# Kernel tuning notes

Hardware: AMD Instinct MI355X
Metric: run time of the kernel (lower is better)

## Reference

```python
import jax, jax.numpy as jnp
import numpy as np

KERNEL_MUL = 2.0
KERNEL_NUM = 5
FIX_SIGMA = None


def setup_inputs() -> dict:
    key = jax.random.key(0)
    k1, k2 = jax.random.split(key)
    source = jax.random.normal(k1, (4096, 64), dtype=jnp.float32)
    target = jax.random.normal(k2, (4096, 64), dtype=jnp.float32)
    return {"source": source, "target": target}


def reference(source, target):
    batch_size = source.shape[0]
    total = jnp.concatenate([source, target], axis=0)  # [2N, D]
    n_samples = total.shape[0]
    sq = jnp.sum(total * total, axis=1)  # [2N]
    L2 = sq[:, None] + sq[None, :] - 2.0 * (total @ total.T)  # [2N, 2N]
    if FIX_SIGMA:
        bandwidth = jnp.asarray(FIX_SIGMA, dtype=L2.dtype)
    else:
        # torch uses L2_distance.data -> detached; no grad through bandwidth
        bandwidth = jax.lax.stop_gradient(jnp.sum(L2)) / (n_samples ** 2 - n_samples)
    bandwidth = bandwidth / (KERNEL_MUL ** (KERNEL_NUM // 2))
    kernels = jnp.zeros_like(L2)
    for i in range(KERNEL_NUM):  # small fixed loop over bandwidths
        kernels = kernels + jnp.exp(-L2 / (bandwidth * (KERNEL_MUL ** i)))
    XX = kernels[:batch_size, :batch_size]
    YY = kernels[batch_size:, batch_size:]
    XY = kernels[:batch_size, batch_size:]
    YX = kernels[batch_size:, :batch_size]
    return jnp.mean(XX + YY - XY - YX)
```

## Files before the change

### kernel.cpp

```cpp
#include <hip/hip_runtime.h>
#include <math.h>

#define N_TOTAL 8192
#define BATCH   4096
#define DIMS    64
#define P1_BLOCKS 256
#define SEG     8
#define NSEG    16
#define NPART   2048


#if defined(__has_builtin)
#if __has_builtin(__builtin_amdgcn_exp2f)
#define EXP2F(x) __builtin_amdgcn_exp2f(x)
#endif
#endif
#ifndef EXP2F
#define EXP2F(x) exp2f(x)
#endif

typedef __attribute__((ext_vector_type(8))) short bf16x8;
typedef __attribute__((ext_vector_type(4))) float f32x4;
typedef __attribute__((ext_vector_type(4))) short s16x4;

__device__ inline short f2bf_rn(float x) {
    unsigned u = __float_as_uint(x);
    unsigned r = (u + 0x7fffu + ((u >> 16) & 1u)) >> 16;
    return (short)r;
}

__global__ __launch_bounds__(256) void pass1_kernel(const float* __restrict__ src,
                                                    const float* __restrict__ tgt,
                                                    double* __restrict__ sqpart,
                                                    double* __restrict__ colpart,
                                                    float* __restrict__ sqbuf,
                                                    short* __restrict__ Xh) {
    __shared__ double cred[4][64];
    __shared__ double sred[4];
    const int lane = threadIdx.x & 63;
    const int wv = threadIdx.x >> 6;
    const int sub = lane >> 4;
    const int k4 = (lane & 15) << 2;
    const int gw = blockIdx.x * 4 + wv;
    const int numWaves = P1_BLOCKS * 4;

    double colacc[4] = {0.0, 0.0, 0.0, 0.0};
    double sqacc = 0.0;

    for (int g = gw; g < N_TOTAL / 4; g += numWaves) {
        int r = g * 4 + sub;
        const float* row = (r < BATCH) ? (src + (size_t)r * DIMS)
                                       : (tgt + (size_t)(r - BATCH) * DIMS);
        float4 v = *(const float4*)(row + k4);
        float xs[4] = {v.x, v.y, v.z, v.w};
        s16x4 h;
        float ssum = 0.f;
        #pragma unroll
        for (int i = 0; i < 4; ++i) {
            h[i] = f2bf_rn(xs[i]);
            colacc[i] += (double)xs[i];
            ssum = fmaf(xs[i], xs[i], ssum);
        }
        *(s16x4*)(Xh + (size_t)r * DIMS + k4) = h;
        ssum += __shfl_xor(ssum, 1, 64);
        ssum += __shfl_xor(ssum, 2, 64);
        ssum += __shfl_xor(ssum, 4, 64);
        ssum += __shfl_xor(ssum, 8, 64);
        if ((lane & 15) == 0) { sqbuf[r] = ssum; sqacc += (double)ssum; }
    }
    #pragma unroll
    for (int i = 0; i < 4; ++i) {
        colacc[i] += __shfl_xor(colacc[i], 16, 64);
        colacc[i] += __shfl_xor(colacc[i], 32, 64);
    }
    sqacc += __shfl_xor(sqacc, 16, 64);
    sqacc += __shfl_xor(sqacc, 32, 64);
    if (lane < 16) {
        #pragma unroll
        for (int i = 0; i < 4; ++i) cred[wv][lane * 4 + i] = colacc[i];
    }
    if (lane == 0) sred[wv] = sqacc;
    __syncthreads();
    if (wv == 0) {
        double c = (cred[0][lane] + cred[1][lane]) + (cred[2][lane] + cred[3][lane]);
        colpart[(size_t)blockIdx.x * 64 + lane] = c;
        if (lane == 0)
            sqpart[blockIdx.x] = (sred[0] + sred[1]) + (sred[2] + sred[3]);
    }
}

__global__ __launch_bounds__(256) void scale_kernel(const double* __restrict__ sqpart,
                                                    const double* __restrict__ colpart,
                                                    float* __restrict__ csp) {
    __shared__ double cred[4][64];
    __shared__ double sred[4];
    const int t = threadIdx.x;
    const int lane = t & 63, w = t >> 6;

    double colacc = 0.0;
    #pragma unroll 4
    for (int b = w; b < P1_BLOCKS; b += 4)
        colacc += colpart[(size_t)b * 64 + lane];
    cred[w][lane] = colacc;

    double sacc = sqpart[t];
    #pragma unroll
    for (int off = 32; off > 0; off >>= 1) sacc += __shfl_xor(sacc, off, 64);
    if (lane == 0) sred[w] = sacc;
    __syncthreads();

    if (w == 0) {
        double colsum = (cred[0][lane] + cred[1][lane])
                      + (cred[2][lane] + cred[3][lane]);
        double vv = colsum * colsum;
        #pragma unroll
        for (int off = 32; off > 0; off >>= 1) vv += __shfl_xor(vv, off, 64);
        if (lane == 0) {
            double sq = (sred[0] + sred[1]) + (sred[2] + sred[3]);
            const double n = (double)N_TOTAL;
            double bw0 = (2.0 * n * sq - 2.0 * vv) / (n * n - n) * 0.25;
            csp[0] = (float)(-1.0 / (bw0 * 0.6931471805599453 * 16.0));
        }
    }
}

__global__ __launch_bounds__(512) void pass2_kernel(const short* __restrict__ Xh,
                                                    const float* __restrict__ sqbuf,
                                                    const float* __restrict__ csp,
                                                    float* __restrict__ partials) {
    const int bc = blockIdx.x;
    const int r0 = blockIdx.y * SEG;
    const int pidx = blockIdx.y * 128 + bc;
    const int t = threadIdx.x;
    if (r0 > bc) {
        if (t == 0) partials[pidx] = 0.f;
        return;
    }
    const int r1 = (bc < r0 + SEG - 1) ? bc : r0 + SEG - 1;

    __shared__ __align__(16) short Bh[64][72];
    __shared__ float s_wred[8];

    const int lane = t & 63, w = t >> 6;
    const int strip = w & 3, ts = w >> 2;
    const int quad = lane >> 4, lrow = lane & 15;

    {
        int row = t >> 3;
        int c8 = (t & 7) << 3;
        size_t gsrc = (size_t)(bc * 64 + row) * DIMS + c8;
        *(s16x4*)&Bh[row][c8]     = *(const s16x4*)(Xh + gsrc);
        *(s16x4*)&Bh[row][c8 + 4] = *(const s16x4*)(Xh + gsrc + 4);
    }
    const float cs = csp[0];
    const float c2 = -2.f * cs;
    float sbc[4];
    #pragma unroll
    for (int j = 0; j < 4; ++j)
        sbc[j] = sqbuf[bc * 64 + j * 16 + lrow] * cs;
    __syncthreads();

    const size_t aoff = (size_t)(strip * 16 + lrow) * DIMS + quad * 8;

    float facc = 0.f;

    for (int r = r0 + ts; r <= r1; r += 2) {
        const size_t abase = (size_t)r * 64 * DIMS + aoff;
        bf16x8 ah0 = *(const bf16x8*)(Xh + abase);
        bf16x8 ah1 = *(const bf16x8*)(Xh + abase + 32);
        float4 csa = *(const float4*)(sqbuf + r * 64 + strip * 16 + quad * 4);

        f32x4 acc[4];
        #pragma unroll
        for (int j = 0; j < 4; ++j) acc[j] = (f32x4){0.f, 0.f, 0.f, 0.f};
        #pragma unroll
        for (int j = 0; j < 4; ++j) {
            const int brow = j * 16 + lrow;
            const int bcol = quad * 8;
            bf16x8 bh0 = *(const bf16x8*)&Bh[brow][bcol];
            bf16x8 bh1 = *(const bf16x8*)&Bh[brow][bcol + 32];
            acc[j] = __builtin_amdgcn_mfma_f32_16x16x32_bf16(ah0, bh0, acc[j], 0, 0, 0);
            acc[j] = __builtin_amdgcn_mfma_f32_16x16x32_bf16(ah1, bh1, acc[j], 0, 0, 0);
        }

        float sac[4] = {csa.x * cs, csa.y * cs, csa.z * cs, csa.w * cs};
        float lsum = 0.f;
        #pragma unroll
        for (int j = 0; j < 4; ++j) {
            #pragma unroll
            for (int p = 0; p < 4; ++p) {
                float t0 = fmaf(acc[j][p], c2, sac[p] + sbc[j]);
                float e4 = EXP2F(t0);
                float e3 = e4 * e4;
                float e2 = e3 * e3;
                float e1 = e2 * e2;
                float e0 = e1 * e1;
                lsum += ((e0 + e1) + (e2 + e3)) + e4;
            }
        }
        float sgn = ((r < 64) == (bc < 64)) ? 1.f : -1.f;
        float wt  = (r == bc) ? 1.f : 2.f;
        facc = fmaf(lsum, sgn * wt, facc);
    }

    #pragma unroll
    for (int off = 32; off > 0; off >>= 1) facc += __shfl_xor(facc, off, 64);
    if (lane == 0) s_wred[w] = facc;
    __syncthreads();
    if (t == 0)
        partials[pidx] = ((s_wred[0] + s_wred[1]) + (s_wred[2] + s_wred[3]))
                       + ((s_wred[4] + s_wred[5]) + (s_wred[6] + s_wred[7]));
}

__global__ __launch_bounds__(256) void finalize_kernel(const float* __restrict__ partials,
                                                       float* __restrict__ out) {
    __shared__ double s_red[4];
    const int t = threadIdx.x;
    const int lane = t & 63, w = t >> 6;
    double acc = 0.0;
    #pragma unroll
    for (int i = 0; i < NPART / 256; ++i)
        acc += (double)partials[t + 256 * i];
    #pragma unroll
    for (int off = 32; off > 0; off >>= 1) acc += __shfl_xor(acc, off, 64);
    if (lane == 0) s_red[w] = acc;
    __syncthreads();
    if (t == 0) {
        double g = (s_red[0] + s_red[1]) + (s_red[2] + s_red[3]);
        out[0] = (float)(g / ((double)BATCH * (double)BATCH));
    }
}

extern "C" void kernel_launch(void* const* d_in, const int* in_sizes, int n_in,
                              void* d_out, int out_size, void* d_ws, size_t ws_size,
                              hipStream_t stream) {
    const float* src = (const float*)d_in[0];
    const float* tgt = (const float*)d_in[1];
    char* ws = (char*)d_ws;
    double* sqpart  = (double*)ws;
    double* colpart = (double*)(ws + 2048);
    float*  csp     = (float*)(ws + 133120);
    float*  parts   = (float*)(ws + 133632);
    float*  sqbuf   = (float*)(ws + 141824);
    short*  Xh      = (short*)(ws + 262144);


    pass1_kernel<<<P1_BLOCKS, 256, 0, stream>>>(src, tgt, sqpart, colpart,
                                                sqbuf, Xh);
    scale_kernel<<<1, 256, 0, stream>>>(sqpart, colpart, csp);

    dim3 grid(128, NSEG);
    pass2_kernel<<<grid, 512, 0, stream>>>(Xh, sqbuf, csp, parts);

    finalize_kernel<<<1, 256, 0, stream>>>(parts, (float*)d_out);
}
```

Measured before the change: 88.30 us.

## Compact triangular pass2 grid, larger row segments, fuse finalize via last-block reduction

Replaces the 128x16 grid, where the lower-triangle blocks exited immediately, with a 1-D grid of 576 blocks that maps directly onto the upper-triangle (column block, row segment) pairs. The mapping puts the largest-index tiles first. Row segments grow from 8 to 16 column tiles, so each block does more work per B tile load. The separate finalize kernel is removed: the last block to finish, found through an atomic counter reset in scale_kernel, sums the partials, which saves one launch and the empty blocks. The cost is a serial tail reduction inside one block, and longer segments may cause load imbalance.

```diff
diff --git a/kernel.cpp b/kernel.cpp
--- a/kernel.cpp
+++ b/kernel.cpp
@@ -5,9 +5,8 @@
 #define BATCH   4096
 #define DIMS    64
 #define P1_BLOCKS 256
-#define SEG     8
-#define NSEG    16
-#define NPART   2048
+#define SEG     16
+#define P2_BLOCKS 576
 
 
 #if defined(__has_builtin)
@@ -91,11 +90,13 @@
 
 __global__ __launch_bounds__(256) void scale_kernel(const double* __restrict__ sqpart,
                                                     const double* __restrict__ colpart,
-                                                    float* __restrict__ csp) {
+                                                    float* __restrict__ csp,
+                                                    int* __restrict__ cnt2) {
     __shared__ double cred[4][64];
     __shared__ double sred[4];
     const int t = threadIdx.x;
     const int lane = t & 63, w = t >> 6;
+    if (t == 0) *cnt2 = 0;
 
     double colacc = 0.0;
     #pragma unroll 4
@@ -127,20 +128,24 @@
 __global__ __launch_bounds__(512) void pass2_kernel(const short* __restrict__ Xh,
                                                     const float* __restrict__ sqbuf,
                                                     const float* __restrict__ csp,
-                                                    float* __restrict__ partials) {
-    const int bc = blockIdx.x;
-    const int r0 = blockIdx.y * SEG;
-    const int pidx = blockIdx.y * 128 + bc;
-    const int t = threadIdx.x;
-    if (r0 > bc) {
-        if (t == 0) partials[pidx] = 0.f;
-        return;
-    }
+                                                    float* __restrict__ partials,
+                                                    int* __restrict__ cnt2,
+                                                    float* __restrict__ out) {
+    const int f = (P2_BLOCKS - 1) - blockIdx.x;
+    int b = 0;
+    while (8 * (b + 1) * (b + 2) <= f) ++b;
+    const int rem = f - 8 * b * (b + 1);
+    const int q = rem / (b + 1);
+    const int bc = 16 * b + q;
+    const int seg = rem - q * (b + 1);
+    const int r0 = seg * SEG;
     const int r1 = (bc < r0 + SEG - 1) ? bc : r0 + SEG - 1;
 
     __shared__ __align__(16) short Bh[64][72];
     __shared__ float s_wred[8];
-
+    __shared__ int s_last;
+
+    const int t = threadIdx.x;
     const int lane = t & 63, w = t >> 6;
     const int strip = w & 3, ts = w >> 2;
     const int quad = lane >> 4, lrow = lane & 15;
@@ -207,27 +212,32 @@
     for (int off = 32; off > 0; off >>= 1) facc += __shfl_xor(facc, off, 64);
     if (lane == 0) s_wred[w] = facc;
     __syncthreads();
-    if (t == 0)
-        partials[pidx] = ((s_wred[0] + s_wred[1]) + (s_wred[2] + s_wred[3]))
-                       + ((s_wred[4] + s_wred[5]) + (s_wred[6] + s_wred[7]));
-}
-
-__global__ __launch_bounds__(256) void finalize_kernel(const float* __restrict__ partials,
-                                                       float* __restrict__ out) {
-    __shared__ double s_red[4];
-    const int t = threadIdx.x;
-    const int lane = t & 63, w = t >> 6;
-    double acc = 0.0;
-    #pragma unroll
-    for (int i = 0; i < NPART / 256; ++i)
-        acc += (double)partials[t + 256 * i];
-    #pragma unroll
-    for (int off = 32; off > 0; off >>= 1) acc += __shfl_xor(acc, off, 64);
-    if (lane == 0) s_red[w] = acc;
-    __syncthreads();
     if (t == 0) {
-        double g = (s_red[0] + s_red[1]) + (s_red[2] + s_red[3]);
-        out[0] = (float)(g / ((double)BATCH * (double)BATCH));
+        partials[blockIdx.x] = ((s_wred[0] + s_wred[1]) + (s_wred[2] + s_wred[3]))
+                             + ((s_wred[4] + s_wred[5]) + (s_wred[6] + s_wred[7]));
+        __threadfence();
+        s_last = (atomicAdd(cnt2, 1) == P2_BLOCKS - 1) ? 1 : 0;
+    }
+    __syncthreads();
+    if (s_last) {
+        __threadfence();
+        double acc = 0.0;
+        #pragma unroll
+        for (int i = 0; i < 2; ++i) {
+            int idx = t + 512 * i;
+            if (idx < P2_BLOCKS)
+                acc += (double)atomicAdd(&partials[idx], 0.f);
+        }
+        #pragma unroll
+        for (int off = 32; off > 0; off >>= 1) acc += __shfl_xor(acc, off, 64);
+        __shared__ double s_red[8];
+        if (lane == 0) s_red[w] = acc;
+        __syncthreads();
+        if (t == 0) {
+            double g = ((s_red[0] + s_red[1]) + (s_red[2] + s_red[3]))
+                     + ((s_red[4] + s_red[5]) + (s_red[6] + s_red[7]));
+            out[0] = (float)(g / ((double)BATCH * (double)BATCH));
+        }
     }
 }
 
@@ -240,6 +250,7 @@
     double* sqpart  = (double*)ws;
     double* colpart = (double*)(ws + 2048);
     float*  csp     = (float*)(ws + 133120);
+    int*    cnt2    = (int*)(ws + 133124);
     float*  parts   = (float*)(ws + 133632);
     float*  sqbuf   = (float*)(ws + 141824);
     short*  Xh      = (short*)(ws + 262144);
@@ -247,10 +258,8 @@
 
     pass1_kernel<<<P1_BLOCKS, 256, 0, stream>>>(src, tgt, sqpart, colpart,
                                                 sqbuf, Xh);
-    scale_kernel<<<1, 256, 0, stream>>>(sqpart, colpart, csp);
-
-    dim3 grid(128, NSEG);
-    pass2_kernel<<<grid, 512, 0, stream>>>(Xh, sqbuf, csp, parts);
-
-    finalize_kernel<<<1, 256, 0, stream>>>(parts, (float*)d_out);
-}
+    scale_kernel<<<1, 256, 0, stream>>>(sqpart, colpart, csp, cnt2);
+
+    pass2_kernel<<<P2_BLOCKS, 512, 0, stream>>>(Xh, sqbuf, csp, parts,
+                                                cnt2, (float*)d_out);
+}
```

Result: slower. 98.46 us (+11.5%).
